# Kernel optimization log

Measured on AMD Instinct MI355X. Metric: run time of the kernel, lower is better.

The kernel has to match this reference:

```python
import jax, jax.numpy as jnp
import numpy as np

E = 8       # expert_number
TOP_K = 2


def setup_inputs() -> dict:
    key = jax.random.key(0)
    ks = jax.random.split(key, 5)
    B, S, D, H = 4, 2048, 1024, 4096
    scale = 0.02
    return {
        "x": jax.random.normal(ks[0], (B, S, D), dtype=jnp.float32),
        "gate_w": jax.random.normal(ks[1], (D, E), dtype=jnp.float32) * scale,
        "gate_b": jnp.zeros((E,), dtype=jnp.float32),
        "w1": jax.random.normal(ks[2], (E, D, H), dtype=jnp.float32) * scale,
        "b1": jnp.zeros((E, H), dtype=jnp.float32),
        "w2": jax.random.normal(ks[3], (E, H, D), dtype=jnp.float32) * scale,
        "b2": jnp.zeros((E, D), dtype=jnp.float32),
    }


def reference(x, gate_w, gate_b, w1, b1, w2, b2):
    B, S, D = x.shape
    h = x.reshape(-1, D)                                   # [T, D]

    # Router: softmax in fp32, top-k, renormalize (matches torch code)
    router_logits = h @ gate_w + gate_b                    # [T, E]
    probs = jax.nn.softmax(router_logits.astype(jnp.float32), axis=-1)
    rw, sel = jax.lax.top_k(probs, TOP_K)                  # [T, K] each
    rw = rw / rw.sum(axis=-1, keepdims=True)
    rw = rw.astype(h.dtype)

    # Per-token combine weight for each expert (0 if not selected): [T, E]
    we = (jax.nn.one_hot(sel, E, dtype=h.dtype) * rw[..., None]).sum(axis=1)

    out = jnp.zeros_like(h)
    for e in range(E):  # fixed small expert count; per-expert GEMM + weighted combine
        mid = jax.nn.gelu(h @ w1[e] + b1[e], approximate=False)  # [T, H]
        ye = mid @ w2[e] + b2[e]                                 # [T, D]
        out = out + we[:, e:e + 1] * ye

    return out.reshape(B, S, D), router_logits
```

## Files before the change

kernel.cpp:

```cpp
#include <hip/hip_runtime.h>
#include <hip/hip_bf16.h>
#include <math.h>

#define T_TOKENS 8192
#define DDIM 1024
#define HDIM 4096
#define NEXP 8
#define CAP 8192

typedef __bf16 bf16;
typedef __bf16 bf16x2 __attribute__((ext_vector_type(2)));
typedef __bf16 bf16x4 __attribute__((ext_vector_type(4)));
typedef __bf16 bf16x8 __attribute__((ext_vector_type(8)));
typedef float  floatx4 __attribute__((ext_vector_type(4)));

__device__ static inline void async_load16(const void* g, void* l)
{
    __builtin_amdgcn_global_load_lds(
        (const __attribute__((address_space(1))) void*)g,
        (__attribute__((address_space(3))) void*)l, 16, 0, 0);
}

__global__ void router_kernel(const float* __restrict__ x,
                              const float* __restrict__ gw,
                              const float* __restrict__ gbias,
                              float* __restrict__ logits_out,
                              int* counts, int* token_of,
                              int* selpack, int* slots, float* wts)
{
    int t = blockIdx.x;
    int l = threadIdx.x;
    const float4* xr = (const float4*)(x + (size_t)t * DDIM);

    float p[NEXP];
#pragma unroll
    for (int e = 0; e < NEXP; ++e) p[e] = 0.f;

#pragma unroll
    for (int it = 0; it < 4; ++it) {
        int d4 = it * 64 + l;
        float4 v = xr[d4];
        float vv[4] = {v.x, v.y, v.z, v.w};
#pragma unroll
        for (int j = 0; j < 4; ++j) {
            const float4* g4 = (const float4*)(gw + (size_t)(d4 * 4 + j) * NEXP);
            float4 ga = g4[0], gb4 = g4[1];
            p[0] += vv[j] * ga.x;  p[1] += vv[j] * ga.y;
            p[2] += vv[j] * ga.z;  p[3] += vv[j] * ga.w;
            p[4] += vv[j] * gb4.x; p[5] += vv[j] * gb4.y;
            p[6] += vv[j] * gb4.z; p[7] += vv[j] * gb4.w;
        }
    }
#pragma unroll
    for (int e = 0; e < NEXP; ++e) {
#pragma unroll
        for (int off = 32; off; off >>= 1) p[e] += __shfl_xor(p[e], off);
        p[e] += gbias[e];
    }
    if (l < NEXP) logits_out[(size_t)t * NEXP + l] = p[l];

    if (l == 0) {
        int e0 = 0;
#pragma unroll
        for (int e = 1; e < NEXP; ++e) if (p[e] > p[e0]) e0 = e;
        int e1 = -1;
#pragma unroll
        for (int e = 0; e < NEXP; ++e) {
            if (e == e0) continue;
            if (e1 < 0 || p[e] > p[e1]) e1 = e;
        }
        float w0 = 1.f / (1.f + expf(p[e1] - p[e0]));
        float w1 = 1.f / (1.f + expf(p[e0] - p[e1]));
        int s0 = atomicAdd(&counts[e0], 1);
        int s1 = atomicAdd(&counts[e1], 1);
        token_of[e0 * CAP + s0] = t;
        token_of[e1 * CAP + s1] = t;
        selpack[t] = e0 | (e1 << 8);
        slots[2 * t]     = s0;
        slots[2 * t + 1] = s1;
        wts[2 * t]     = w0;
        wts[2 * t + 1] = w1;
    }
}

__global__ void offsets_kernel(const int* __restrict__ counts, int* __restrict__ offsets)
{
    if (threadIdx.x == 0) {
        int a = 0;
#pragma unroll
        for (int e = 0; e < NEXP; ++e) { offsets[e] = a; a += counts[e]; }
        offsets[NEXP] = a;
    }
}

__global__ void gather_kernel(const float* __restrict__ x,
                              const int* __restrict__ counts,
                              const int* __restrict__ offsets,
                              const int* __restrict__ token_of,
                              bf16* __restrict__ xg)
{
    int e = blockIdx.y, s = blockIdx.x;
    if (s >= counts[e]) return;
    int t   = token_of[e * CAP + s];
    int row = offsets[e] + s;
    const float4* src = (const float4*)(x + (size_t)t * DDIM);
    bf16x4* dst = (bf16x4*)(xg + (size_t)row * DDIM);
    int l = threadIdx.x;
#pragma unroll
    for (int it = 0; it < 4; ++it) {
        float4 v = src[it * 64 + l];
        bf16x4 b;
        b[0] = (bf16)v.x; b[1] = (bf16)v.y; b[2] = (bf16)v.z; b[3] = (bf16)v.w;
        dst[it * 64 + l] = b;
    }
}

__global__ void transpose_cvt_kernel(const float* __restrict__ in,
                                     bf16* __restrict__ out, int R, int C)
{
    __shared__ bf16 tile[32][66];
    int e = blockIdx.z;
    const float* src = in + (size_t)e * R * C;
    bf16* dst = out + (size_t)e * R * C;
    int c0 = blockIdx.x * 32, r0 = blockIdx.y * 64;
    int tx = threadIdx.x, ty = threadIdx.y;
#pragma unroll
    for (int j = 0; j < 8; ++j) {
        int rr = ty + j * 8;
        tile[tx][rr] = (bf16)src[(size_t)(r0 + rr) * C + c0 + tx];
    }
    __syncthreads();
#pragma unroll
    for (int j = 0; j < 4; ++j) {
        int cc = ty + j * 8;
        int rr = tx * 2;
        bf16x2 v;
        v[0] = tile[cc][rr];
        v[1] = tile[cc][rr + 1];
        *(bf16x2*)(dst + (size_t)(c0 + cc) * R + r0 + rr) = v;
    }
}

template<int KTOT>
__device__ static inline void stage_tile(const bf16* __restrict__ gbase,
                                         bf16* lds, int wave, int lane, int valid)
{
#pragma unroll
    for (int it = 0; it < 4; ++it) {
        int rbase = wave * 32 + it * 8;
        int rloc  = rbase + (lane >> 3);
        int grow  = rloc < valid ? rloc : (valid - 1);
        int chunk = (lane & 7) ^ (rloc & 7);
        const bf16* g = gbase + (size_t)grow * KTOT + chunk * 8;
        async_load16(g, lds + rbase * 64);
    }
}

template<int KTOT, int NTOT, bool DOGELU, typename OutT>
__global__ __launch_bounds__(256, 4)
void moe_gemm(const bf16* __restrict__ Abase, const bf16* __restrict__ Bbase,
              const float* __restrict__ bias, OutT* __restrict__ Out,
              const int* __restrict__ counts, const int* __restrict__ offsets)
{
    int e = blockIdx.z;
    int cnt = counts[e];
    int rows_done = blockIdx.x * 128;
    if (rows_done >= cnt) return;
    int valid = cnt - rows_done; if (valid > 128) valid = 128;
    int row0 = offsets[e] + rows_done;
    int n0 = blockIdx.y * 128;

    const bf16* A = Abase + (size_t)row0 * KTOT;
    const bf16* B = Bbase + (size_t)e * NTOT * KTOT + (size_t)n0 * KTOT;
    const float* bvec = bias + (size_t)e * NTOT + n0;

    __shared__ __align__(16) bf16 As[128 * 64];
    __shared__ __align__(16) bf16 Bs[128 * 64];

    int tid = threadIdx.x;
    int lane = tid & 63, wave = tid >> 6;
    int wr = wave >> 1, wc = wave & 1;
    int m16 = lane & 15, quad = lane >> 4;
    int swz = m16 & 7;

    floatx4 acc[4][4];
#pragma unroll
    for (int i = 0; i < 4; ++i)
#pragma unroll
        for (int j = 0; j < 4; ++j)
#pragma unroll
            for (int r = 0; r < 4; ++r) acc[i][j][r] = 0.f;

    for (int k0 = 0; k0 < KTOT; k0 += 64) {
        stage_tile<KTOT>(A + k0, As, wave, lane, valid);
        stage_tile<KTOT>(B + k0, Bs, wave, lane, 128);
        __syncthreads();
#pragma unroll
        for (int ks = 0; ks < 64; ks += 32) {
            int cbase = (ks >> 3) + quad;
            int pchunk = (cbase ^ swz) * 8;
            bf16x8 af[4], bfr[4];
#pragma unroll
            for (int i = 0; i < 4; ++i)
                af[i] = *(const bf16x8*)(&As[(wr * 64 + i * 16 + m16) * 64 + pchunk]);
#pragma unroll
            for (int j = 0; j < 4; ++j)
                bfr[j] = *(const bf16x8*)(&Bs[(wc * 64 + j * 16 + m16) * 64 + pchunk]);
#pragma unroll
            for (int i = 0; i < 4; ++i)
#pragma unroll
                for (int j = 0; j < 4; ++j)
                    acc[i][j] = __builtin_amdgcn_mfma_f32_16x16x32_bf16(
                        af[i], bfr[j], acc[i][j], 0, 0, 0);
        }
        __syncthreads();
    }

#pragma unroll
    for (int i = 0; i < 4; ++i) {
#pragma unroll
        for (int r = 0; r < 4; ++r) {
            int lrow = wr * 64 + i * 16 + quad * 4 + r;
            if (lrow >= valid) continue;
            size_t orow = (size_t)(row0 + lrow) * NTOT + n0;
#pragma unroll
            for (int j = 0; j < 4; ++j) {
                int lcol = wc * 64 + j * 16 + m16;
                float v = acc[i][j][r] + bvec[lcol];
                if (DOGELU)
                    v = 0.5f * v * (1.f + erff(v * 0.70710678118654752f));
                Out[orow + lcol] = (OutT)v;
            }
        }
    }
}

__global__ void combine_kernel(const float* __restrict__ y,
                               const int* __restrict__ offsets,
                               const int* __restrict__ selpack,
                               const int* __restrict__ slots,
                               const float* __restrict__ wts,
                               float* __restrict__ out)
{
    int t = blockIdx.x;
    int sp = selpack[t];
    int e0 = sp & 0xff, e1 = (sp >> 8) & 0xff;
    int p0 = offsets[e0] + slots[2 * t];
    int p1 = offsets[e1] + slots[2 * t + 1];
    float w0 = wts[2 * t], w1 = wts[2 * t + 1];
    const float4* y0 = (const float4*)(y + (size_t)p0 * DDIM);
    const float4* y1 = (const float4*)(y + (size_t)p1 * DDIM);
    float4* o = (float4*)(out + (size_t)t * DDIM);
    int tid = threadIdx.x;
    float4 a = y0[tid], b = y1[tid];
    float4 rr;
    rr.x = w0 * a.x + w1 * b.x;
    rr.y = w0 * a.y + w1 * b.y;
    rr.z = w0 * a.z + w1 * b.z;
    rr.w = w0 * a.w + w1 * b.w;
    o[tid] = rr;
}

extern "C" void kernel_launch(void* const* d_in, const int* in_sizes, int n_in,
                              void* d_out, int out_size, void* d_ws, size_t ws_size,
                              hipStream_t stream)
{
    (void)in_sizes; (void)n_in; (void)out_size; (void)ws_size;
    const float* x  = (const float*)d_in[0];
    const float* gw = (const float*)d_in[1];
    const float* gb = (const float*)d_in[2];
    const float* w1 = (const float*)d_in[3];
    const float* b1 = (const float*)d_in[4];
    const float* w2 = (const float*)d_in[5];
    const float* b2 = (const float*)d_in[6];
    float* out    = (float*)d_out;
    float* logits = out + (size_t)T_TOKENS * DDIM;

    char* ws = (char*)d_ws;
    const size_t MB = 1024 * 1024;
    int*   counts   = (int*)(ws + 0);
    int*   offsets  = (int*)(ws + 256);
    int*   selpack  = (int*)(ws + 512);
    int*   slots    = (int*)(ws + 512 + 32 * 1024);
    float* wts      = (float*)(ws + 512 + 96 * 1024);
    int*   token_of = (int*)(ws + 512 + 160 * 1024);
    bf16*  xg  = (bf16*)(ws + 1 * MB);
    bf16*  w1b = (bf16*)(ws + 33 * MB);
    bf16*  w2b = (bf16*)(ws + 97 * MB);
    bf16*  mid = (bf16*)(ws + 161 * MB);
    float* y   = (float*)(ws + 289 * MB);

    hipMemsetAsync(counts, 0, 32, stream);

    router_kernel<<<T_TOKENS, 64, 0, stream>>>(x, gw, gb, logits, counts,
                                               token_of, selpack, slots, wts);
    offsets_kernel<<<1, 64, 0, stream>>>(counts, offsets);
    gather_kernel<<<dim3(CAP, NEXP), 64, 0, stream>>>(x, counts, offsets, token_of, xg);
    transpose_cvt_kernel<<<dim3(HDIM / 32, DDIM / 64, NEXP), dim3(32, 8), 0, stream>>>(
        w1, w1b, DDIM, HDIM);
    transpose_cvt_kernel<<<dim3(DDIM / 32, HDIM / 64, NEXP), dim3(32, 8), 0, stream>>>(
        w2, w2b, HDIM, DDIM);
    moe_gemm<DDIM, HDIM, true, bf16><<<dim3(64, HDIM / 128, NEXP), 256, 0, stream>>>(
        xg, w1b, b1, mid, counts, offsets);
    moe_gemm<HDIM, DDIM, false, float><<<dim3(64, DDIM / 128, NEXP), 256, 0, stream>>>(
        mid, w2b, b2, y, counts, offsets);
    combine_kernel<<<T_TOKENS, 256, 0, stream>>>(y, offsets, selpack, slots, wts, out);
}
```

Before: 1.176 ms.

## Compact MoE GEMM tile list, widen transpose, flatten gather, approximate GELU

The offsets kernel now builds a compact list of (expert, row) 128-row tiles, so the grouped GEMMs launch a flat grid of at most 136 tiles instead of 64×8 blocks where most exit early. The gather kernel maps four rows per 256-thread block over the packed row space, and the weight transpose now uses float4 loads and 16-byte bf16x8 stores over 64×64 tiles. The exact erf GELU is replaced by a sigmoid-form exp2/rcp approximation, which cuts epilogue cost but changes numerics slightly.

```diff
diff --git a/kernel.cpp b/kernel.cpp
--- a/kernel.cpp
+++ b/kernel.cpp
@@ -7,6 +7,7 @@
 #define HDIM 4096
 #define NEXP 8
 #define CAP 8192
+#define MAXTILES 136
 
 typedef __bf16 bf16;
 typedef __bf16 bf16x2 __attribute__((ext_vector_type(2)));
@@ -83,29 +84,37 @@
     }
 }
 
-__global__ void offsets_kernel(const int* __restrict__ counts, int* __restrict__ offsets)
+__global__ void offsets_kernel(const int* __restrict__ counts,
+                               int* __restrict__ offsets,
+                               int* __restrict__ tiles,
+                               int* __restrict__ ntiles)
 {
     if (threadIdx.x == 0) {
-        int a = 0;
-#pragma unroll
-        for (int e = 0; e < NEXP; ++e) { offsets[e] = a; a += counts[e]; }
+        int a = 0, nt = 0;
+        for (int e = 0; e < NEXP; ++e) {
+            offsets[e] = a;
+            for (int r = 0; r < counts[e]; r += 128)
+                tiles[nt++] = (e << 24) | (a + r);
+            a += counts[e];
+        }
         offsets[NEXP] = a;
+        *ntiles = nt;
     }
 }
 
 __global__ void gather_kernel(const float* __restrict__ x,
-                              const int* __restrict__ counts,
                               const int* __restrict__ offsets,
                               const int* __restrict__ token_of,
                               bf16* __restrict__ xg)
 {
-    int e = blockIdx.y, s = blockIdx.x;
-    if (s >= counts[e]) return;
-    int t   = token_of[e * CAP + s];
-    int row = offsets[e] + s;
+    int row = blockIdx.x * 4 + (threadIdx.x >> 6);
+    int l = threadIdx.x & 63;
+    int e = 0;
+#pragma unroll
+    for (int i = 1; i < NEXP; ++i) e += (row >= offsets[i]);
+    int t = token_of[e * CAP + (row - offsets[e])];
     const float4* src = (const float4*)(x + (size_t)t * DDIM);
     bf16x4* dst = (bf16x4*)(xg + (size_t)row * DDIM);
-    int l = threadIdx.x;
 #pragma unroll
     for (int it = 0; it < 4; ++it) {
         float4 v = src[it * 64 + l];
@@ -118,26 +127,30 @@
 __global__ void transpose_cvt_kernel(const float* __restrict__ in,
                                      bf16* __restrict__ out, int R, int C)
 {
-    __shared__ bf16 tile[32][66];
+    __shared__ bf16 tile[64][68];
     int e = blockIdx.z;
     const float* src = in + (size_t)e * R * C;
     bf16* dst = out + (size_t)e * R * C;
-    int c0 = blockIdx.x * 32, r0 = blockIdx.y * 64;
-    int tx = threadIdx.x, ty = threadIdx.y;
-#pragma unroll
-    for (int j = 0; j < 8; ++j) {
-        int rr = ty + j * 8;
-        tile[tx][rr] = (bf16)src[(size_t)(r0 + rr) * C + c0 + tx];
+    int r0 = blockIdx.y * 64, c0 = blockIdx.x * 64;
+    int t = threadIdx.x;
+    int lr = t >> 4, c4 = t & 15;
+#pragma unroll
+    for (int it = 0; it < 4; ++it) {
+        int r = lr + it * 16;
+        float4 v = *(const float4*)(src + (size_t)(r0 + r) * C + c0 + c4 * 4);
+        bf16x4 b;
+        b[0] = (bf16)v.x; b[1] = (bf16)v.y; b[2] = (bf16)v.z; b[3] = (bf16)v.w;
+        *(bf16x4*)(&tile[r][c4 * 4]) = b;
     }
     __syncthreads();
-#pragma unroll
-    for (int j = 0; j < 4; ++j) {
-        int cc = ty + j * 8;
-        int rr = tx * 2;
-        bf16x2 v;
-        v[0] = tile[cc][rr];
-        v[1] = tile[cc][rr + 1];
-        *(bf16x2*)(dst + (size_t)(c0 + cc) * R + r0 + rr) = v;
+    int oc = t >> 3, rseg = (t & 7) * 8;
+#pragma unroll
+    for (int it = 0; it < 2; ++it) {
+        int c = oc + it * 32;
+        bf16x8 v;
+#pragma unroll
+        for (int j = 0; j < 8; ++j) v[j] = tile[rseg + j][c];
+        *(bf16x8*)(dst + (size_t)(c0 + c) * R + r0 + rseg) = v;
     }
 }
 
@@ -156,18 +169,24 @@
     }
 }
 
+__device__ static inline float fast_gelu(float v)
+{
+    float z = v * (2.302236479f + 0.1029451170f * v * v);
+    float ex = __builtin_amdgcn_exp2f(z);
+    return v * ex * __builtin_amdgcn_rcpf(ex + 1.f);
+}
+
 template<int KTOT, int NTOT, bool DOGELU, typename OutT>
 __global__ __launch_bounds__(256, 4)
 void moe_gemm(const bf16* __restrict__ Abase, const bf16* __restrict__ Bbase,
               const float* __restrict__ bias, OutT* __restrict__ Out,
-              const int* __restrict__ counts, const int* __restrict__ offsets)
-{
-    int e = blockIdx.z;
-    int cnt = counts[e];
-    int rows_done = blockIdx.x * 128;
-    if (rows_done >= cnt) return;
-    int valid = cnt - rows_done; if (valid > 128) valid = 128;
-    int row0 = offsets[e] + rows_done;
+              const int* __restrict__ tiles, const int* __restrict__ ntiles,
+              const int* __restrict__ offsets)
+{
+    if (blockIdx.x >= *ntiles) return;
+    int info = tiles[blockIdx.x];
+    int e = info >> 24, row0 = info & 0xffffff;
+    int valid = offsets[e + 1] - row0; if (valid > 128) valid = 128;
     int n0 = blockIdx.y * 128;
 
     const bf16* A = Abase + (size_t)row0 * KTOT;
@@ -227,8 +246,7 @@
             for (int j = 0; j < 4; ++j) {
                 int lcol = wc * 64 + j * 16 + m16;
                 float v = acc[i][j][r] + bvec[lcol];
-                if (DOGELU)
-                    v = 0.5f * v * (1.f + erff(v * 0.70710678118654752f));
+                if (DOGELU) v = fast_gelu(v);
                 Out[orow + lcol] = (OutT)v;
             }
         }
@@ -280,10 +298,12 @@
     const size_t MB = 1024 * 1024;
     int*   counts   = (int*)(ws + 0);
     int*   offsets  = (int*)(ws + 256);
-    int*   selpack  = (int*)(ws + 512);
-    int*   slots    = (int*)(ws + 512 + 32 * 1024);
-    float* wts      = (float*)(ws + 512 + 96 * 1024);
-    int*   token_of = (int*)(ws + 512 + 160 * 1024);
+    int*   tiles    = (int*)(ws + 512);
+    int*   ntiles   = (int*)(ws + 512 + 1024);
+    int*   selpack  = (int*)(ws + 4096);
+    int*   slots    = (int*)(ws + 4096 + 32 * 1024);
+    float* wts      = (float*)(ws + 4096 + 96 * 1024);
+    int*   token_of = (int*)(ws + 4096 + 160 * 1024);
     bf16*  xg  = (bf16*)(ws + 1 * MB);
     bf16*  w1b = (bf16*)(ws + 33 * MB);
     bf16*  w2b = (bf16*)(ws + 97 * MB);
@@ -294,15 +314,15 @@
 
     router_kernel<<<T_TOKENS, 64, 0, stream>>>(x, gw, gb, logits, counts,
                                                token_of, selpack, slots, wts);
-    offsets_kernel<<<1, 64, 0, stream>>>(counts, offsets);
-    gather_kernel<<<dim3(CAP, NEXP), 64, 0, stream>>>(x, counts, offsets, token_of, xg);
-    transpose_cvt_kernel<<<dim3(HDIM / 32, DDIM / 64, NEXP), dim3(32, 8), 0, stream>>>(
+    offsets_kernel<<<1, 64, 0, stream>>>(counts, offsets, tiles, ntiles);
+    gather_kernel<<<2 * T_TOKENS / 4, 256, 0, stream>>>(x, offsets, token_of, xg);
+    transpose_cvt_kernel<<<dim3(HDIM / 64, DDIM / 64, NEXP), 256, 0, stream>>>(
         w1, w1b, DDIM, HDIM);
-    transpose_cvt_kernel<<<dim3(DDIM / 32, HDIM / 64, NEXP), dim3(32, 8), 0, stream>>>(
+    transpose_cvt_kernel<<<dim3(DDIM / 64, HDIM / 64, NEXP), 256, 0, stream>>>(
         w2, w2b, HDIM, DDIM);
-    moe_gemm<DDIM, HDIM, true, bf16><<<dim3(64, HDIM / 128, NEXP), 256, 0, stream>>>(
-        xg, w1b, b1, mid, counts, offsets);
-    moe_gemm<HDIM, DDIM, false, float><<<dim3(64, DDIM / 128, NEXP), 256, 0, stream>>>(
-        mid, w2b, b2, y, counts, offsets);
+    moe_gemm<DDIM, HDIM, true, bf16><<<dim3(MAXTILES, HDIM / 128), 256, 0, stream>>>(
+        xg, w1b, b1, mid, tiles, ntiles, offsets);
+    moe_gemm<HDIM, DDIM, false, float><<<dim3(MAXTILES, DDIM / 128), 256, 0, stream>>>(
+        mid, w2b, b2, y, tiles, ntiles, offsets);
     combine_kernel<<<T_TOKENS, 256, 0, stream>>>(y, offsets, selpack, slots, wts, out);
 }
```

After: 970.5 us. -17.4%, faster.
